# Optimization experiments

Measured on AMD Instinct MI355X. Metric: run time of the kernel, lower is better.

The kernel has to match this reference:

```python
import jax, jax.numpy as jnp
import numpy as np

B, S = 64, 200
DK = 32           # d_k = d_a = d_e
NQ = 4096         # n_question
NE = 20000        # n_exercise
NAT = 2000
NIT = 2000


def _xavier(k, shape):
    a = float(np.sqrt(6.0 / (shape[0] + shape[1])))
    return jax.random.uniform(k, shape, jnp.float32, -a, a)


def setup_inputs() -> dict:
    key = jax.random.key(0)
    ks = jax.random.split(key, 24)
    d = {}
    d['e_data'] = jax.random.randint(ks[0], (B, S), 0, NE)
    d['at_data'] = jax.random.randint(ks[1], (B, S), 0, NAT)
    d['it_data'] = jax.random.randint(ks[2], (B, S), 0, NIT)
    d['a_data'] = jax.random.randint(ks[3], (B, S), 0, 2).astype(jnp.float32)
    # binary Q-matrix: ~64 skills per exercise on average
    d['q_matrix'] = (jax.random.uniform(ks[4], (NE + 10, NQ + 1)) < (64.0 / NQ)).astype(jnp.float32)
    d['E_e'] = _xavier(ks[5], (NE + 10, DK))
    d['E_at'] = _xavier(ks[6], (NAT + 10, DK))
    d['E_it'] = _xavier(ks[7], (NIT + 10, DK))
    d['W1'] = _xavier(ks[8], (DK, 3 * DK)); d['b1'] = jnp.zeros((DK,), jnp.float32)
    d['W2'] = _xavier(ks[9], (DK, 4 * DK)); d['b2'] = jnp.zeros((DK,), jnp.float32)
    d['W3'] = _xavier(ks[10], (DK, 4 * DK)); d['b3'] = jnp.zeros((DK,), jnp.float32)
    d['W4'] = _xavier(ks[11], (DK, 3 * DK)); d['b4'] = jnp.zeros((DK,), jnp.float32)
    d['W5'] = _xavier(ks[12], (DK, 2 * DK)); d['b5'] = jnp.zeros((DK,), jnp.float32)
    d['h0'] = _xavier(ks[13], (NQ + 1, DK))
    return d


def _forward(e_data, at_data, it_data, a_data, q_matrix, E_e, E_at, E_it,
             W1, b1, W2, b2, W3, b3, W4, b4, W5, b5, h0):
    e_emb = E_e[e_data]                    # [B,S,DK]
    at_emb = E_at[at_data]                 # [B,S,DK]
    it_emb = E_it[it_data]                 # [B,S,DK]
    a_rep = jnp.broadcast_to(a_data[:, :, None], (B, S, DK))  # repeat answer to d_a
    all_learning = jnp.einsum('bsf,kf->bsk', jnp.concatenate([e_emb, at_emb, a_rep], -1), W1) + b1

    h_pre0 = jnp.broadcast_to(h0[None], (B, NQ + 1, DK))
    h_tilde0 = jnp.einsum('bn,bnd->bd', q_matrix[e_data[:, 0]], h_pre0)
    W4h, W4l, W4i = W4[:, :DK], W4[:, DK:2 * DK], W4[:, 2 * DK:]

    def step(carry, xs):
        learning_pre, h_pre, h_tilde_pre = carry
        e_t, it, learning, e_next_emb, e_next = xs
        q_e = q_matrix[e_t]                               # [B,NQ+1] gather
        x = jnp.concatenate([learning_pre, it, learning, h_tilde_pre], -1)  # [B,4DK]
        lg = jnp.tanh(x @ W2.T + b2)
        gl = jax.nn.sigmoid(x @ W3.T + b3)
        LG = gl * (lg + 1.0) * 0.5                        # [B,DK]
        LG_tilde = q_e[:, :, None] * LG[:, None, :]       # scatter (outer product), dropout off (eval)
        gamma_f = jax.nn.sigmoid(h_pre @ W4h.T + (LG @ W4l.T + it @ W4i.T + b4)[:, None, :])
        h = LG_tilde + gamma_f * h_pre                    # [B,NQ+1,DK]
        h_tilde = jnp.einsum('bn,bnd->bd', q_matrix[e_next], h)
        y = jax.nn.sigmoid(jnp.concatenate([e_next_emb, h_tilde], -1) @ W5.T + b5).sum(-1) / DK
        return (learning, h, h_tilde), y

    xs = (e_data[:, :-1].T,
          jnp.swapaxes(it_emb[:, :-1], 0, 1),
          jnp.swapaxes(all_learning[:, :-1], 0, 1),
          jnp.swapaxes(e_emb[:, 1:], 0, 1),
          e_data[:, 1:].T)
    init = (jnp.zeros((B, DK), jnp.float32), h_pre0, h_tilde0)
    _, ys = jax.lax.scan(step, init, xs)                  # ys: [S-1,B]
    pred = jnp.concatenate([jnp.zeros((B, 1), jnp.float32), ys.T], axis=1)
    return pred


def reference(e_data, at_data, it_data, a_data, q_matrix, E_e, E_at, E_it,
              W1, b1, W2, b2, W3, b3, W4, b4, W5, b5, h0):
    return _forward(e_data, at_data, it_data, a_data, q_matrix, E_e, E_at, E_it,
                    W1, b1, W2, b2, W3, b3, W4, b4, W5, b5, h0)
```

## Files before the change

kernel.cpp:

```cpp
#include <hip/hip_runtime.h>

#define Bv    64
#define Sv    200
#define DKv   32
#define NQ1v  4097
#define NWG   8
#define TPB   256
#define ROWS  2
#define NSTEP 199

typedef unsigned long long u64;

__device__ __forceinline__ float fsig(float x) {
  return __builtin_amdgcn_rcpf(1.0f + __builtin_amdgcn_exp2f(x * -1.4426950408889634f));
}
__device__ __forceinline__ float ftanh_(float x) {
  return fmaf(2.0f, fsig(2.0f * x), -1.0f);
}
__device__ __forceinline__ u64 packvt(float v, unsigned tag) {
  return ((u64)tag << 32) | (u64)__float_as_uint(v);
}

__global__ void lpkt_init(float* out) {
  int i = threadIdx.x;
  if (i < Bv) out[i * Sv] = 0.0f;
}

__global__ __launch_bounds__(TPB, 2) void lpkt_main(
    const int* __restrict__ e_data, const int* __restrict__ at_data,
    const int* __restrict__ it_data, const float* __restrict__ a_data,
    const float* __restrict__ q_matrix,
    const float* __restrict__ E_e, const float* __restrict__ E_at, const float* __restrict__ E_it,
    const float* __restrict__ W1, const float* __restrict__ b1,
    const float* __restrict__ W2, const float* __restrict__ b2,
    const float* __restrict__ W3, const float* __restrict__ b3,
    const float* __restrict__ W4, const float* __restrict__ b4,
    const float* __restrict__ W5, const float* __restrict__ b5,
    const float* __restrict__ h0, float* __restrict__ out,
    u64* __restrict__ partial)
{
  const int tid = threadIdx.x;
  const int wg  = blockIdx.x & (NWG - 1);
  const int b   = blockIdx.x / NWG;
  const int k   = tid & 31;
  const int p   = tid >> 5;
  const int nbase = wg * (TPB * ROWS);

  __shared__ __align__(16) float xw_lds[96];
  __shared__ __align__(16) float it_lds[DKv];
  __shared__ __align__(16) float lcA[DKv], lcB[DKv];
  __shared__ __align__(16) float ht_lds[DKv];
  __shared__ __align__(16) float LG_lds[DKv];
  __shared__ __align__(16) float c_lds[DKv];
  __shared__ __align__(16) float red[8][DKv];
  __shared__ __align__(16) float red2[8][DKv];
  __shared__ float ht_part[DKv];
  __shared__ __align__(16) float h49[DKv];
  __shared__ float W2T[128 * DKv];
  __shared__ float W3T[128 * DKv];

  for (int idx = tid; idx < 128 * DKv; idx += TPB) {
    int kk = idx >> 7, j = idx & 127;
    W2T[j * DKv + kk] = W2[idx];
    W3T[j * DKv + kk] = W3[idx];
  }
  if (tid < DKv) { ht_part[tid] = 0.0f; lcB[tid] = 0.0f; }
  if (wg == 0 && tid < DKv) h49[tid] = h0[4096 * DKv + tid];

  float h[ROWS][DKv];
#pragma unroll
  for (int r = 0; r < ROWS; r++) {
    const float4* hp = (const float4*)(h0 + (size_t)(nbase + r * TPB + tid) * DKv);
#pragma unroll
    for (int i = 0; i < 8; i++) {
      float4 v = hp[i];
      h[r][4*i] = v.x; h[r][4*i+1] = v.y; h[r][4*i+2] = v.z; h[r][4*i+3] = v.w;
    }
  }
  const int e0 = e_data[b * Sv];
  const float* q0 = q_matrix + (size_t)e0 * NQ1v;
  float qc[ROWS];
#pragma unroll
  for (int r = 0; r < ROWS; r++) qc[r] = q0[nbase + r * TPB + tid];
  float qc49 = (wg == 0 && tid < DKv) ? q0[4096] : 0.0f;
  __syncthreads();

#pragma unroll
  for (int r = 0; r < ROWS; r++) {
    if (qc[r] != 0.0f) {
#pragma unroll
      for (int kk = 0; kk < DKv; kk++) atomicAdd(&ht_part[kk], h[r][kk]);
    }
  }
  if (wg == 0 && tid < DKv && qc49 != 0.0f) atomicAdd(&ht_part[tid], h49[tid]);
  __syncthreads();
  if (tid < DKv)
    __hip_atomic_store(&partial[((size_t)(1 % 3) * Bv + b) * (NWG * DKv) + wg * DKv + tid],
                       packvt(ht_part[tid], 1u), __ATOMIC_RELAXED, __HIP_MEMORY_SCOPE_AGENT);

  for (int t = 0; t < NSTEP; t++) {
    float* lc_cur  = (t & 1) ? lcB : lcA;
    float* lc_prev = (t & 1) ? lcA : lcB;
    const unsigned tau_g = (unsigned)(t + 1);
    const unsigned tau_p = (unsigned)(t + 2);

    const int ecur  = e_data[b * Sv + t];
    const int enext = e_data[b * Sv + t + 1];
    const int atc   = at_data[b * Sv + t];
    const int itc   = it_data[b * Sv + t];
    const float av  = a_data[b * Sv + t];
    const float* qnr = q_matrix + (size_t)enext * NQ1v;
    float qn[ROWS];
#pragma unroll
    for (int r = 0; r < ROWS; r++) qn[r] = qnr[nbase + r * TPB + tid];
    float qn49 = (wg == 0 && tid < DKv) ? qnr[4096] : 0.0f;

    if (tid < 96)
      xw_lds[tid] = (tid < 32) ? E_e[(size_t)ecur * DKv + tid]
                  : (tid < 64) ? E_at[(size_t)atc * DKv + (tid - 32)] : av;
    else if (tid < 128)
      it_lds[tid - 96] = E_it[(size_t)itc * DKv + (tid - 96)];

    float acc[ROWS][DKv];
#pragma unroll
    for (int kk = 0; kk < DKv; kk++) {
      float a0 = 0.0f, a1 = 0.0f;
#pragma unroll
      for (int d = 0; d < DKv; d += 4) {
        float4 w = *(const float4*)&W4[kk * 96 + d];
        a0 = fmaf(w.x, h[0][d+0], a0); a1 = fmaf(w.x, h[1][d+0], a1);
        a0 = fmaf(w.y, h[0][d+1], a0); a1 = fmaf(w.y, h[1][d+1], a1);
        a0 = fmaf(w.z, h[0][d+2], a0); a1 = fmaf(w.z, h[1][d+2], a1);
        a0 = fmaf(w.w, h[0][d+3], a0); a1 = fmaf(w.w, h[1][d+3], a1);
      }
      acc[0][kk] = a0; acc[1][kk] = a1;
    }
    __syncthreads();

    if (tid >= 32 && tid < 64) {
      const int kx = tid - 32;
      float s = b1[kx];
      const float4* wp = (const float4*)&W1[kx * 96];
      const float4* xp = (const float4*)xw_lds;
#pragma unroll
      for (int i = 0; i < 24; i++) {
        float4 w = wp[i]; float4 x = xp[i];
        s = fmaf(x.x, w.x, s); s = fmaf(x.y, w.y, s);
        s = fmaf(x.z, w.z, s); s = fmaf(x.w, w.w, s);
      }
      lc_cur[kx] = s;
    }
    if (tid < DKv) {
      const u64* pb = partial + ((size_t)(tau_g % 3) * Bv + b) * (NWG * DKv) + tid;
      u64 v[NWG];
      for (;;) {
        bool ok = true;
#pragma unroll
        for (int w2 = 0; w2 < NWG; w2++) {
          v[w2] = __hip_atomic_load(&pb[w2 * DKv], __ATOMIC_RELAXED, __HIP_MEMORY_SCOPE_AGENT);
          ok = ok && ((unsigned)(v[w2] >> 32) == tau_g);
        }
        if (ok) break;
        __builtin_amdgcn_s_sleep(2);
      }
      float s = 0.0f;
#pragma unroll
      for (int w2 = 0; w2 < NWG; w2++) s += __uint_as_float((unsigned)v[w2]);
      ht_lds[tid] = s;
    }
    __syncthreads();

    {
      const int seg = p >> 1;
      const float* sp = (seg == 0) ? lc_prev : (seg == 1) ? it_lds
                      : (seg == 2) ? lc_cur  : ht_lds;
      const int off = (p & 1) * 16;
      float xv[16];
#pragma unroll
      for (int i = 0; i < 4; i++) {
        float4 v = ((const float4*)(sp + off))[i];
        xv[4*i] = v.x; xv[4*i+1] = v.y; xv[4*i+2] = v.z; xv[4*i+3] = v.w;
      }
      float s2 = 0.0f, s3 = 0.0f;
      const int jb = 16 * p;
#pragma unroll
      for (int i = 0; i < 16; i++) {
        s2 = fmaf(xv[i], W2T[(jb + i) * DKv + k], s2);
        s3 = fmaf(xv[i], W3T[(jb + i) * DKv + k], s3);
      }
      red[p][k] = s2; red2[p][k] = s3;
    }
    __syncthreads();

    if (tid < DKv) {
      float s2 = b2[tid], s3 = b3[tid];
#pragma unroll
      for (int pp = 0; pp < 8; pp++) { s2 += red[pp][tid]; s3 += red2[pp][tid]; }
      LG_lds[tid] = fsig(s3) * (ftanh_(s2) + 1.0f) * 0.5f;
    } else if (tid < 64) ht_part[tid - 32] = 0.0f;
    __syncthreads();

    {
      const float* up = (p < 4) ? (LG_lds + 8 * p) : (it_lds + 8 * (p - 4));
      const float4* wp = (const float4*)&W4[k * 96 + 32 + 8 * p];
      float4 w0 = wp[0], w1 = wp[1];
      float pc = 0.0f;
      pc = fmaf(up[0], w0.x, pc); pc = fmaf(up[1], w0.y, pc);
      pc = fmaf(up[2], w0.z, pc); pc = fmaf(up[3], w0.w, pc);
      pc = fmaf(up[4], w1.x, pc); pc = fmaf(up[5], w1.y, pc);
      pc = fmaf(up[6], w1.z, pc); pc = fmaf(up[7], w1.w, pc);
      red[p][k] = pc;
    }
    if (wg == 0 && t >= 1 && tid >= 64 && tid < 128) {
      const int p2 = p - 2;
      const float* zs = (p2 == 0) ? xw_lds : ht_lds;
      const float4* wp = (const float4*)&W5[k * 64 + 32 * p2];
      float acc5 = 0.0f;
#pragma unroll
      for (int i = 0; i < 8; i++) {
        float4 w = wp[i]; float4 z = ((const float4*)zs)[i];
        acc5 = fmaf(z.x, w.x, acc5); acc5 = fmaf(z.y, w.y, acc5);
        acc5 = fmaf(z.z, w.z, acc5); acc5 = fmaf(z.w, w.w, acc5);
      }
      red2[p2][k] = acc5;
    }
    __syncthreads();

    if (tid < DKv) {
      float s = b4[tid];
#pragma unroll
      for (int pp = 0; pp < 8; pp++) s += red[pp][tid];
      c_lds[tid] = s;
    } else if (wg == 0 && t >= 1 && tid < 64) {
      const int kx = tid - 32;
      float s = fsig(b5[kx] + red2[0][kx] + red2[1][kx]);
#pragma unroll
      for (int m = 1; m < 32; m <<= 1) s += __shfl_xor(s, m);
      if (tid == 32) out[b * Sv + t] = s * (1.0f / DKv);
    }
    __syncthreads();

    {
      float c_r[DKv], lg_r[DKv];
#pragma unroll
      for (int i = 0; i < 8; i++) {
        float4 cv = ((const float4*)c_lds)[i];
        float4 gv = ((const float4*)LG_lds)[i];
        c_r[4*i] = cv.x; c_r[4*i+1] = cv.y; c_r[4*i+2] = cv.z; c_r[4*i+3] = cv.w;
        lg_r[4*i] = gv.x; lg_r[4*i+1] = gv.y; lg_r[4*i+2] = gv.z; lg_r[4*i+3] = gv.w;
      }
#pragma unroll
      for (int r = 0; r < ROWS; r++) {
        const float qcr = qc[r];
#pragma unroll
        for (int kk = 0; kk < DKv; kk++) {
          float g = fsig(acc[r][kk] + c_r[kk]);
          h[r][kk] = fmaf(g, h[r][kk], qcr * lg_r[kk]);
        }
        if (qn[r] != 0.0f) {
#pragma unroll
          for (int kk = 0; kk < DKv; kk++) atomicAdd(&ht_part[kk], h[r][kk]);
        }
        qc[r] = qn[r];
      }
    }
    if (wg == 0 && tid < DKv) {
      float hh[DKv];
#pragma unroll
      for (int i = 0; i < 8; i++) {
        float4 v = ((const float4*)h49)[i];
        hh[4*i] = v.x; hh[4*i+1] = v.y; hh[4*i+2] = v.z; hh[4*i+3] = v.w;
      }
      float a = c_lds[tid];
#pragma unroll
      for (int d = 0; d < DKv; d += 4) {
        float4 w = *(const float4*)&W4[tid * 96 + d];
        a = fmaf(w.x, hh[d+0], a); a = fmaf(w.y, hh[d+1], a);
        a = fmaf(w.z, hh[d+2], a); a = fmaf(w.w, hh[d+3], a);
      }
      float hn = fmaf(fsig(a), h49[tid], qc49 * LG_lds[tid]);
      h49[tid] = hn;
      if (qn49 != 0.0f) atomicAdd(&ht_part[tid], hn);
      qc49 = qn49;
    }
    __syncthreads();

    if (tid < DKv)
      __hip_atomic_store(&partial[((size_t)(tau_p % 3) * Bv + b) * (NWG * DKv) + wg * DKv + tid],
                         packvt(ht_part[tid], tau_p), __ATOMIC_RELAXED, __HIP_MEMORY_SCOPE_AGENT);
  }

  if (wg == 0) {
    const unsigned tau_f = (unsigned)(NSTEP + 1);
    if (tid < DKv) {
      const u64* pb = partial + ((size_t)(tau_f % 3) * Bv + b) * (NWG * DKv) + tid;
      u64 v[NWG];
      for (;;) {
        bool ok = true;
#pragma unroll
        for (int w2 = 0; w2 < NWG; w2++) {
          v[w2] = __hip_atomic_load(&pb[w2 * DKv], __ATOMIC_RELAXED, __HIP_MEMORY_SCOPE_AGENT);
          ok = ok && ((unsigned)(v[w2] >> 32) == tau_f);
        }
        if (ok) break;
        __builtin_amdgcn_s_sleep(2);
      }
      float s = 0.0f;
#pragma unroll
      for (int w2 = 0; w2 < NWG; w2++) s += __uint_as_float((unsigned)v[w2]);
      ht_lds[tid] = s;
      xw_lds[tid] = E_e[(size_t)e_data[b * Sv + 199] * DKv + tid];
    }
    __syncthreads();
    if (tid >= 64 && tid < 128) {
      const int p2 = p - 2;
      const float* zs = (p2 == 0) ? xw_lds : ht_lds;
      const float4* wp = (const float4*)&W5[k * 64 + 32 * p2];
      float acc5 = 0.0f;
#pragma unroll
      for (int i = 0; i < 8; i++) {
        float4 w = wp[i]; float4 z = ((const float4*)zs)[i];
        acc5 = fmaf(z.x, w.x, acc5); acc5 = fmaf(z.y, w.y, acc5);
        acc5 = fmaf(z.z, w.z, acc5); acc5 = fmaf(z.w, w.w, acc5);
      }
      red2[p2][k] = acc5;
    }
    __syncthreads();
    if (tid >= 32 && tid < 64) {
      const int kx = tid - 32;
      float s = fsig(b5[kx] + red2[0][kx] + red2[1][kx]);
#pragma unroll
      for (int m = 1; m < 32; m <<= 1) s += __shfl_xor(s, m);
      if (tid == 32) out[b * Sv + 199] = s * (1.0f / DKv);
    }
  }
}

extern "C" void kernel_launch(void* const* d_in, const int* in_sizes, int n_in,
                              void* d_out, int out_size, void* d_ws, size_t ws_size,
                              hipStream_t stream) {
  const int*   e_data   = (const int*)d_in[0];
  const int*   at_data  = (const int*)d_in[1];
  const int*   it_data  = (const int*)d_in[2];
  const float* a_data   = (const float*)d_in[3];
  const float* q_matrix = (const float*)d_in[4];
  const float* E_e      = (const float*)d_in[5];
  const float* E_at     = (const float*)d_in[6];
  const float* E_it     = (const float*)d_in[7];
  const float* W1 = (const float*)d_in[8];
  const float* b1 = (const float*)d_in[9];
  const float* W2 = (const float*)d_in[10];
  const float* b2 = (const float*)d_in[11];
  const float* W3 = (const float*)d_in[12];
  const float* b3 = (const float*)d_in[13];
  const float* W4 = (const float*)d_in[14];
  const float* b4 = (const float*)d_in[15];
  const float* W5 = (const float*)d_in[16];
  const float* b5 = (const float*)d_in[17];
  const float* h0 = (const float*)d_in[18];
  float* out = (float*)d_out;

  u64* partial = (u64*)d_ws;

  lpkt_init<<<1, 64, 0, stream>>>(out);
  lpkt_main<<<dim3(Bv * NWG), dim3(TPB), 0, stream>>>(
      e_data, at_data, it_data, a_data, q_matrix, E_e, E_at, E_it,
      W1, b1, W2, b2, W3, b3, W4, b4, W5, b5, h0, out, partial);
}
```

Before: 5.190 ms.

## Cache weights in LDS, use atomic RMW for cross-block flags, split warp roles

```diff
diff --git a/kernel.cpp b/kernel.cpp
--- a/kernel.cpp
+++ b/kernel.cpp
@@ -19,6 +19,12 @@
 }
 __device__ __forceinline__ u64 packvt(float v, unsigned tag) {
   return ((u64)tag << 32) | (u64)__float_as_uint(v);
+}
+__device__ __forceinline__ u64 fresh_read(u64* p) {
+  return __hip_atomic_fetch_add(p, 0ull, __ATOMIC_RELAXED, __HIP_MEMORY_SCOPE_AGENT);
+}
+__device__ __forceinline__ void fresh_write(u64* p, u64 v) {
+  (void)__hip_atomic_exchange(p, v, __ATOMIC_RELAXED, __HIP_MEMORY_SCOPE_AGENT);
 }
 
 __global__ void lpkt_init(float* out) {
@@ -46,6 +52,11 @@
   const int p   = tid >> 5;
   const int nbase = wg * (TPB * ROWS);
 
+  __shared__ float W23T[128 * 64];
+  __shared__ __align__(16) float W1L[32 * 100];
+  __shared__ __align__(16) float W4L[32 * 100];
+  __shared__ __align__(16) float W5L[32 * 68];
+  __shared__ float bL[5 * 32];
   __shared__ __align__(16) float xw_lds[96];
   __shared__ __align__(16) float it_lds[DKv];
   __shared__ __align__(16) float lcA[DKv], lcB[DKv];
@@ -56,13 +67,25 @@
   __shared__ __align__(16) float red2[8][DKv];
   __shared__ float ht_part[DKv];
   __shared__ __align__(16) float h49[DKv];
-  __shared__ float W2T[128 * DKv];
-  __shared__ float W3T[128 * DKv];
-
-  for (int idx = tid; idx < 128 * DKv; idx += TPB) {
-    int kk = idx >> 7, j = idx & 127;
-    W2T[j * DKv + kk] = W2[idx];
-    W3T[j * DKv + kk] = W3[idx];
+
+  for (int idx = tid; idx < 128 * 32; idx += TPB) {
+    int j = idx & 127, kk = idx >> 7;
+    W23T[j * 64 + 2 * kk]     = W2[kk * 128 + j];
+    W23T[j * 64 + 2 * kk + 1] = W3[kk * 128 + j];
+  }
+  for (int idx = tid; idx < 32 * 96; idx += TPB) {
+    int r = idx / 96, c = idx % 96;
+    W1L[r * 100 + c] = W1[idx];
+    W4L[r * 100 + c] = W4[idx];
+  }
+  for (int idx = tid; idx < 32 * 64; idx += TPB) {
+    int r = idx >> 6, c = idx & 63;
+    W5L[r * 68 + c] = W5[idx];
+  }
+  if (tid < 32) {
+    bL[0 * 32 + tid] = b1[tid]; bL[1 * 32 + tid] = b2[tid];
+    bL[2 * 32 + tid] = b3[tid]; bL[3 * 32 + tid] = b4[tid];
+    bL[4 * 32 + tid] = b5[tid];
   }
   if (tid < DKv) { ht_part[tid] = 0.0f; lcB[tid] = 0.0f; }
   if (wg == 0 && tid < DKv) h49[tid] = h0[4096 * DKv + tid];
@@ -95,8 +118,8 @@
   if (wg == 0 && tid < DKv && qc49 != 0.0f) atomicAdd(&ht_part[tid], h49[tid]);
   __syncthreads();
   if (tid < DKv)
-    __hip_atomic_store(&partial[((size_t)(1 % 3) * Bv + b) * (NWG * DKv) + wg * DKv + tid],
-                       packvt(ht_part[tid], 1u), __ATOMIC_RELAXED, __HIP_MEMORY_SCOPE_AGENT);
+    fresh_write(&partial[((size_t)(1 % 3) * Bv + b) * (NWG * DKv) + wg * DKv + tid],
+                packvt(ht_part[tid], 1u));
 
   for (int t = 0; t < NSTEP; t++) {
     float* lc_cur  = (t & 1) ? lcB : lcA;
@@ -137,10 +160,27 @@
     }
     __syncthreads();
 
-    if (tid >= 32 && tid < 64) {
-      const int kx = tid - 32;
-      float s = b1[kx];
-      const float4* wp = (const float4*)&W1[kx * 96];
+    if (tid < DKv) {
+      u64* pb = partial + ((size_t)(tau_g % 3) * Bv + b) * (NWG * DKv) + tid;
+      u64 v[NWG];
+      for (;;) {
+        bool ok = true;
+#pragma unroll
+        for (int w2 = 0; w2 < NWG; w2++) {
+          v[w2] = fresh_read(&pb[w2 * DKv]);
+          ok = ok && ((unsigned)(v[w2] >> 32) == tau_g);
+        }
+        if (ok) break;
+        __builtin_amdgcn_s_sleep(2);
+      }
+      float s = 0.0f;
+#pragma unroll
+      for (int w2 = 0; w2 < NWG; w2++) s += __uint_as_float((unsigned)v[w2]);
+      ht_lds[tid] = s;
+    } else if (tid >= 64 && tid < 96) {
+      const int kx = tid - 64;
+      float s = bL[0 * 32 + kx];
+      const float4* wp = (const float4*)&W1L[kx * 100];
       const float4* xp = (const float4*)xw_lds;
 #pragma unroll
       for (int i = 0; i < 24; i++) {
@@ -149,24 +189,6 @@
         s = fmaf(x.z, w.z, s); s = fmaf(x.w, w.w, s);
       }
       lc_cur[kx] = s;
-    }
-    if (tid < DKv) {
-      const u64* pb = partial + ((size_t)(tau_g % 3) * Bv + b) * (NWG * DKv) + tid;
-      u64 v[NWG];
-      for (;;) {
-        bool ok = true;
-#pragma unroll
-        for (int w2 = 0; w2 < NWG; w2++) {
-          v[w2] = __hip_atomic_load(&pb[w2 * DKv], __ATOMIC_RELAXED, __HIP_MEMORY_SCOPE_AGENT);
-          ok = ok && ((unsigned)(v[w2] >> 32) == tau_g);
-        }
-        if (ok) break;
-        __builtin_amdgcn_s_sleep(2);
-      }
-      float s = 0.0f;
-#pragma unroll
-      for (int w2 = 0; w2 < NWG; w2++) s += __uint_as_float((unsigned)v[w2]);
-      ht_lds[tid] = s;
     }
     __syncthreads();
 
@@ -185,24 +207,25 @@
       const int jb = 16 * p;
 #pragma unroll
       for (int i = 0; i < 16; i++) {
-        s2 = fmaf(xv[i], W2T[(jb + i) * DKv + k], s2);
-        s3 = fmaf(xv[i], W3T[(jb + i) * DKv + k], s3);
+        float2 w = *(const float2*)&W23T[(jb + i) * 64 + 2 * k];
+        s2 = fmaf(xv[i], w.x, s2);
+        s3 = fmaf(xv[i], w.y, s3);
       }
       red[p][k] = s2; red2[p][k] = s3;
     }
     __syncthreads();
 
     if (tid < DKv) {
-      float s2 = b2[tid], s3 = b3[tid];
+      float s2 = bL[1 * 32 + tid], s3 = bL[2 * 32 + tid];
 #pragma unroll
       for (int pp = 0; pp < 8; pp++) { s2 += red[pp][tid]; s3 += red2[pp][tid]; }
       LG_lds[tid] = fsig(s3) * (ftanh_(s2) + 1.0f) * 0.5f;
-    } else if (tid < 64) ht_part[tid - 32] = 0.0f;
+    } else if (tid >= 128 && tid < 160) ht_part[tid - 128] = 0.0f;
     __syncthreads();
 
     {
       const float* up = (p < 4) ? (LG_lds + 8 * p) : (it_lds + 8 * (p - 4));
-      const float4* wp = (const float4*)&W4[k * 96 + 32 + 8 * p];
+      const float4* wp = (const float4*)&W4L[k * 100 + 32 + 8 * p];
       float4 w0 = wp[0], w1 = wp[1];
       float pc = 0.0f;
       pc = fmaf(up[0], w0.x, pc); pc = fmaf(up[1], w0.y, pc);
@@ -214,7 +237,7 @@
     if (wg == 0 && t >= 1 && tid >= 64 && tid < 128) {
       const int p2 = p - 2;
       const float* zs = (p2 == 0) ? xw_lds : ht_lds;
-      const float4* wp = (const float4*)&W5[k * 64 + 32 * p2];
+      const float4* wp = (const float4*)&W5L[k * 68 + 32 * p2];
       float acc5 = 0.0f;
 #pragma unroll
       for (int i = 0; i < 8; i++) {
@@ -227,16 +250,16 @@
     __syncthreads();
 
     if (tid < DKv) {
-      float s = b4[tid];
+      float s = bL[3 * 32 + tid];
 #pragma unroll
       for (int pp = 0; pp < 8; pp++) s += red[pp][tid];
       c_lds[tid] = s;
-    } else if (wg == 0 && t >= 1 && tid < 64) {
-      const int kx = tid - 32;
-      float s = fsig(b5[kx] + red2[0][kx] + red2[1][kx]);
+    } else if (wg == 0 && t >= 1 && tid >= 96 && tid < 128) {
+      const int kx = tid - 96;
+      float s = fsig(bL[4 * 32 + kx] + red2[0][kx] + red2[1][kx]);
 #pragma unroll
       for (int m = 1; m < 32; m <<= 1) s += __shfl_xor(s, m);
-      if (tid == 32) out[b * Sv + t] = s * (1.0f / DKv);
+      if (tid == 96) out[b * Sv + t] = s * (1.0f / DKv);
     }
     __syncthreads();
 
@@ -274,7 +297,7 @@
       float a = c_lds[tid];
 #pragma unroll
       for (int d = 0; d < DKv; d += 4) {
-        float4 w = *(const float4*)&W4[tid * 96 + d];
+        float4 w = *(const float4*)&W4L[tid * 100 + d];
         a = fmaf(w.x, hh[d+0], a); a = fmaf(w.y, hh[d+1], a);
         a = fmaf(w.z, hh[d+2], a); a = fmaf(w.w, hh[d+3], a);
       }
@@ -286,20 +309,20 @@
     __syncthreads();
 
     if (tid < DKv)
-      __hip_atomic_store(&partial[((size_t)(tau_p % 3) * Bv + b) * (NWG * DKv) + wg * DKv + tid],
-                         packvt(ht_part[tid], tau_p), __ATOMIC_RELAXED, __HIP_MEMORY_SCOPE_AGENT);
+      fresh_write(&partial[((size_t)(tau_p % 3) * Bv + b) * (NWG * DKv) + wg * DKv + tid],
+                  packvt(ht_part[tid], tau_p));
   }
 
   if (wg == 0) {
     const unsigned tau_f = (unsigned)(NSTEP + 1);
     if (tid < DKv) {
-      const u64* pb = partial + ((size_t)(tau_f % 3) * Bv + b) * (NWG * DKv) + tid;
+      u64* pb = partial + ((size_t)(tau_f % 3) * Bv + b) * (NWG * DKv) + tid;
       u64 v[NWG];
       for (;;) {
         bool ok = true;
 #pragma unroll
         for (int w2 = 0; w2 < NWG; w2++) {
-          v[w2] = __hip_atomic_load(&pb[w2 * DKv], __ATOMIC_RELAXED, __HIP_MEMORY_SCOPE_AGENT);
+          v[w2] = fresh_read(&pb[w2 * DKv]);
           ok = ok && ((unsigned)(v[w2] >> 32) == tau_f);
         }
         if (ok) break;
@@ -315,7 +338,7 @@
     if (tid >= 64 && tid < 128) {
       const int p2 = p - 2;
       const float* zs = (p2 == 0) ? xw_lds : ht_lds;
-      const float4* wp = (const float4*)&W5[k * 64 + 32 * p2];
+      const float4* wp = (const float4*)&W5L[k * 68 + 32 * p2];
       float acc5 = 0.0f;
 #pragma unroll
       for (int i = 0; i < 8; i++) {
@@ -326,12 +349,12 @@
       red2[p2][k] = acc5;
     }
     __syncthreads();
-    if (tid >= 32 && tid < 64) {
-      const int kx = tid - 32;
-      float s = fsig(b5[kx] + red2[0][kx] + red2[1][kx]);
+    if (tid >= 96 && tid < 128) {
+      const int kx = tid - 96;
+      float s = fsig(bL[4 * 32 + kx] + red2[0][kx] + red2[1][kx]);
 #pragma unroll
       for (int m = 1; m < 32; m <<= 1) s += __shfl_xor(s, m);
-      if (tid == 32) out[b * Sv + 199] = s * (1.0f / DKv);
+      if (tid == 96) out[b * Sv + 199] = s * (1.0f / DKv);
     }
   }
 }
```

After: 4.904 ms. 1.06x faster.

## Restructure recurrent step: 512 threads, one row each, single-wave small matmuls

Applied to the files above, without the earlier changes.

```diff
diff --git a/kernel.cpp b/kernel.cpp
--- a/kernel.cpp
+++ b/kernel.cpp
@@ -5,8 +5,7 @@
 #define DKv   32
 #define NQ1v  4097
 #define NWG   8
-#define TPB   256
-#define ROWS  2
+#define TPB   512
 #define NSTEP 199
 
 typedef unsigned long long u64;
@@ -19,6 +18,12 @@
 }
 __device__ __forceinline__ u64 packvt(float v, unsigned tag) {
   return ((u64)tag << 32) | (u64)__float_as_uint(v);
+}
+__device__ __forceinline__ u64 fresh_read(u64* p) {
+  return __hip_atomic_fetch_add(p, 0ull, __ATOMIC_RELAXED, __HIP_MEMORY_SCOPE_AGENT);
+}
+__device__ __forceinline__ void fresh_write(u64* p, u64 v) {
+  (void)__hip_atomic_exchange(p, v, __ATOMIC_RELAXED, __HIP_MEMORY_SCOPE_AGENT);
 }
 
 __global__ void lpkt_init(float* out) {
@@ -26,7 +31,7 @@
   if (i < Bv) out[i * Sv] = 0.0f;
 }
 
-__global__ __launch_bounds__(TPB, 2) void lpkt_main(
+__global__ __launch_bounds__(TPB, 4) void lpkt_main(
     const int* __restrict__ e_data, const int* __restrict__ at_data,
     const int* __restrict__ it_data, const float* __restrict__ a_data,
     const float* __restrict__ q_matrix,
@@ -39,300 +44,241 @@
     const float* __restrict__ h0, float* __restrict__ out,
     u64* __restrict__ partial)
 {
-  const int tid = threadIdx.x;
-  const int wg  = blockIdx.x & (NWG - 1);
-  const int b   = blockIdx.x / NWG;
-  const int k   = tid & 31;
-  const int p   = tid >> 5;
-  const int nbase = wg * (TPB * ROWS);
-
-  __shared__ __align__(16) float xw_lds[96];
-  __shared__ __align__(16) float it_lds[DKv];
-  __shared__ __align__(16) float lcA[DKv], lcB[DKv];
-  __shared__ __align__(16) float ht_lds[DKv];
-  __shared__ __align__(16) float LG_lds[DKv];
-  __shared__ __align__(16) float c_lds[DKv];
-  __shared__ __align__(16) float red[8][DKv];
-  __shared__ __align__(16) float red2[8][DKv];
-  __shared__ float ht_part[DKv];
+  const int tid  = threadIdx.x;
+  const int b    = blockIdx.x & 63;
+  const int wg   = blockIdx.x >> 6;
+  const int lane = tid & 63;
+  const int wave = tid >> 6;
+  const int row  = wg * TPB + tid;
+
+  __shared__ float W2T[128 * 33], W3T[128 * 33];
+  __shared__ float W1T[96 * 33];
+  __shared__ float W4cT[64 * 33];
+  __shared__ float W4hT[32 * 33];
+  __shared__ float W5T[64 * 33];
+  __shared__ float bs[5 * 32];
+  __shared__ __align__(16) float lc_s[2][DKv];
+  __shared__ __align__(16) float ht_s[DKv];
+  __shared__ __align__(16) float LG_s[DKv], c_s[DKv];
+  __shared__ __align__(16) float ht_part[2][DKv];
   __shared__ __align__(16) float h49[DKv];
-  __shared__ float W2T[128 * DKv];
-  __shared__ float W3T[128 * DKv];
-
-  for (int idx = tid; idx < 128 * DKv; idx += TPB) {
-    int kk = idx >> 7, j = idx & 127;
-    W2T[j * DKv + kk] = W2[idx];
-    W3T[j * DKv + kk] = W3[idx];
-  }
-  if (tid < DKv) { ht_part[tid] = 0.0f; lcB[tid] = 0.0f; }
+
+  for (int idx = tid; idx < 128 * 32; idx += TPB) {
+    int i = idx & 127, j = idx >> 7;
+    W2T[i * 33 + j] = W2[j * 128 + i];
+    W3T[i * 33 + j] = W3[j * 128 + i];
+  }
+  for (int idx = tid; idx < 32 * 96; idx += TPB) {
+    int j = idx / 96, d = idx % 96;
+    W1T[d * 33 + j] = W1[idx];
+    float v = W4[idx];
+    if (d < 32) W4hT[d * 33 + j] = v;
+    else        W4cT[(d - 32) * 33 + j] = v;
+  }
+  for (int idx = tid; idx < 32 * 64; idx += TPB) {
+    int j = idx >> 6, i = idx & 63;
+    W5T[i * 33 + j] = W5[idx];
+  }
+  if (tid < 32) {
+    bs[tid] = b1[tid]; bs[32 + tid] = b2[tid]; bs[64 + tid] = b3[tid];
+    bs[96 + tid] = b4[tid]; bs[128 + tid] = b5[tid];
+    ht_part[0][tid] = 0.0f; ht_part[1][tid] = 0.0f;
+    lc_s[0][tid] = 0.0f; lc_s[1][tid] = 0.0f;
+  }
   if (wg == 0 && tid < DKv) h49[tid] = h0[4096 * DKv + tid];
 
-  float h[ROWS][DKv];
-#pragma unroll
-  for (int r = 0; r < ROWS; r++) {
-    const float4* hp = (const float4*)(h0 + (size_t)(nbase + r * TPB + tid) * DKv);
+  float h[DKv];
+  {
+    const float4* hp = (const float4*)(h0 + (size_t)row * DKv);
 #pragma unroll
     for (int i = 0; i < 8; i++) {
       float4 v = hp[i];
-      h[r][4*i] = v.x; h[r][4*i+1] = v.y; h[r][4*i+2] = v.z; h[r][4*i+3] = v.w;
-    }
-  }
-  const int e0 = e_data[b * Sv];
-  const float* q0 = q_matrix + (size_t)e0 * NQ1v;
-  float qc[ROWS];
-#pragma unroll
-  for (int r = 0; r < ROWS; r++) qc[r] = q0[nbase + r * TPB + tid];
-  float qc49 = (wg == 0 && tid < DKv) ? q0[4096] : 0.0f;
+      h[4*i] = v.x; h[4*i+1] = v.y; h[4*i+2] = v.z; h[4*i+3] = v.w;
+    }
+  }
+  float qc = q_matrix[(size_t)e_data[b * Sv] * NQ1v + row];
+  float qc49 = 0.0f;
+  if (wg == 0 && wave == 0 && lane < DKv)
+    qc49 = q_matrix[(size_t)e_data[b * Sv] * NQ1v + 4096];
   __syncthreads();
 
-#pragma unroll
-  for (int r = 0; r < ROWS; r++) {
-    if (qc[r] != 0.0f) {
-#pragma unroll
-      for (int kk = 0; kk < DKv; kk++) atomicAdd(&ht_part[kk], h[r][kk]);
-    }
-  }
-  if (wg == 0 && tid < DKv && qc49 != 0.0f) atomicAdd(&ht_part[tid], h49[tid]);
+  if (qc != 0.0f) {
+#pragma unroll
+    for (int kk = 0; kk < DKv; kk++) atomicAdd(&ht_part[1][kk], h[kk]);
+  }
+  if (wg == 0 && wave == 0 && lane < DKv && qc49 != 0.0f)
+    atomicAdd(&ht_part[1][lane], h49[lane]);
   __syncthreads();
-  if (tid < DKv)
-    __hip_atomic_store(&partial[((size_t)(1 % 3) * Bv + b) * (NWG * DKv) + wg * DKv + tid],
-                       packvt(ht_part[tid], 1u), __ATOMIC_RELAXED, __HIP_MEMORY_SCOPE_AGENT);
+  if (wave == 0 && lane < DKv) {
+    fresh_write(&partial[((size_t)(1 % 3) * Bv + b) * (NWG * DKv) + wg * DKv + lane],
+                packvt(ht_part[1][lane], 1u));
+    ht_part[1][lane] = 0.0f;
+  }
 
   for (int t = 0; t < NSTEP; t++) {
-    float* lc_cur  = (t & 1) ? lcB : lcA;
-    float* lc_prev = (t & 1) ? lcA : lcB;
+    const int par = t & 1;
     const unsigned tau_g = (unsigned)(t + 1);
     const unsigned tau_p = (unsigned)(t + 2);
 
-    const int ecur  = e_data[b * Sv + t];
-    const int enext = e_data[b * Sv + t + 1];
-    const int atc   = at_data[b * Sv + t];
-    const int itc   = it_data[b * Sv + t];
-    const float av  = a_data[b * Sv + t];
-    const float* qnr = q_matrix + (size_t)enext * NQ1v;
-    float qn[ROWS];
-#pragma unroll
-    for (int r = 0; r < ROWS; r++) qn[r] = qnr[nbase + r * TPB + tid];
-    float qn49 = (wg == 0 && tid < DKv) ? qnr[4096] : 0.0f;
-
-    if (tid < 96)
-      xw_lds[tid] = (tid < 32) ? E_e[(size_t)ecur * DKv + tid]
-                  : (tid < 64) ? E_at[(size_t)atc * DKv + (tid - 32)] : av;
-    else if (tid < 128)
-      it_lds[tid - 96] = E_it[(size_t)itc * DKv + (tid - 96)];
-
-    float acc[ROWS][DKv];
+    const int ec  = e_data[b * Sv + t];
+    const int atc = at_data[b * Sv + t];
+    const int itc = it_data[b * Sv + t];
+    const float av = a_data[b * Sv + t];
+    const float* eerow = E_e  + (size_t)ec  * DKv;
+    const float* atrow = E_at + (size_t)atc * DKv;
+    const float* itrow = E_it + (size_t)itc * DKv;
+
+    const float* qnr = q_matrix + (size_t)e_data[b * Sv + t + 1] * NQ1v;
+    float qn = qnr[row];
+    float qn49 = 0.0f;
+    if (wg == 0 && wave == 0 && lane < DKv) qn49 = qnr[4096];
+
+    float acc[DKv];
 #pragma unroll
     for (int kk = 0; kk < DKv; kk++) {
-      float a0 = 0.0f, a1 = 0.0f;
+      float a = 0.0f;
 #pragma unroll
       for (int d = 0; d < DKv; d += 4) {
         float4 w = *(const float4*)&W4[kk * 96 + d];
-        a0 = fmaf(w.x, h[0][d+0], a0); a1 = fmaf(w.x, h[1][d+0], a1);
-        a0 = fmaf(w.y, h[0][d+1], a0); a1 = fmaf(w.y, h[1][d+1], a1);
-        a0 = fmaf(w.z, h[0][d+2], a0); a1 = fmaf(w.z, h[1][d+2], a1);
-        a0 = fmaf(w.w, h[0][d+3], a0); a1 = fmaf(w.w, h[1][d+3], a1);
+        a = fmaf(w.x, h[d+0], a); a = fmaf(w.y, h[d+1], a);
+        a = fmaf(w.z, h[d+2], a); a = fmaf(w.w, h[d+3], a);
       }
-      acc[0][kk] = a0; acc[1][kk] = a1;
+      acc[kk] = a;
+    }
+
+    if (wave == 0) {
+      if (lane < 32) {
+        u64* pb = partial + ((size_t)(tau_g % 3) * Bv + b) * (NWG * DKv) + lane;
+        u64 v[NWG];
+        for (;;) {
+          bool ok = true;
+#pragma unroll
+          for (int w2 = 0; w2 < NWG; w2++) {
+            v[w2] = fresh_read(&pb[w2 * DKv]);
+            ok = ok && ((unsigned)(v[w2] >> 32) == tau_g);
+          }
+          if (ok) break;
+          __builtin_amdgcn_s_sleep(2);
+        }
+        float s = 0.0f;
+#pragma unroll
+        for (int w2 = 0; w2 < NWG; w2++) s += __uint_as_float((unsigned)v[w2]);
+        ht_s[lane] = s;
+      } else {
+        const int jx = lane - 32;
+        float s = bs[jx];
+#pragma unroll
+        for (int i = 0; i < 32; i++) s = fmaf(eerow[i], W1T[i * 33 + jx], s);
+#pragma unroll
+        for (int i = 0; i < 32; i++) s = fmaf(atrow[i], W1T[(32 + i) * 33 + jx], s);
+#pragma unroll
+        for (int i = 0; i < 32; i++) s = fmaf(av,       W1T[(64 + i) * 33 + jx], s);
+        lc_s[par][jx] = s;
+      }
     }
     __syncthreads();
 
-    if (tid >= 32 && tid < 64) {
-      const int kx = tid - 32;
-      float s = b1[kx];
-      const float4* wp = (const float4*)&W1[kx * 96];
-      const float4* xp = (const float4*)xw_lds;
-#pragma unroll
-      for (int i = 0; i < 24; i++) {
-        float4 w = wp[i]; float4 x = xp[i];
-        s = fmaf(x.x, w.x, s); s = fmaf(x.y, w.y, s);
-        s = fmaf(x.z, w.z, s); s = fmaf(x.w, w.w, s);
+    float LGreg = 0.0f, creg = 0.0f;
+    if (wave == 0) {
+      const int jx = lane & 31;
+      float s = (lane < 32) ? bs[32 + jx] : bs[64 + jx];
+      const float* WT = (lane < 32) ? W2T : W3T;
+#pragma unroll
+      for (int i = 0; i < 32; i++) s = fmaf(lc_s[1 - par][i], WT[i * 33 + jx], s);
+#pragma unroll
+      for (int i = 0; i < 32; i++) s = fmaf(itrow[i],         WT[(32 + i) * 33 + jx], s);
+#pragma unroll
+      for (int i = 0; i < 32; i++) s = fmaf(lc_s[par][i],     WT[(64 + i) * 33 + jx], s);
+#pragma unroll
+      for (int i = 0; i < 32; i++) s = fmaf(ht_s[i],          WT[(96 + i) * 33 + jx], s);
+      float v = (lane < 32) ? ftanh_(s) : fsig(s);
+      float pr = __shfl_xor(v, 32);
+      LGreg = (lane < 32) ? pr * (v + 1.0f) * 0.5f : v * (pr + 1.0f) * 0.5f;
+      if (lane < 32) {
+        LG_s[lane] = LGreg;
+        float c = bs[96 + lane];
+#pragma unroll
+        for (int d = 0; d < 32; d++)
+          c = fmaf(__shfl(LGreg, d), W4cT[d * 33 + lane], c);
+#pragma unroll
+        for (int d = 0; d < 32; d++)
+          c = fmaf(itrow[d], W4cT[(32 + d) * 33 + lane], c);
+        creg = c; c_s[lane] = c;
+      } else if (wg == 0 && t >= 1) {
+        float y = bs[128 + jx];
+#pragma unroll
+        for (int i = 0; i < 32; i++) y = fmaf(eerow[i], W5T[i * 33 + jx], y);
+#pragma unroll
+        for (int i = 0; i < 32; i++) y = fmaf(ht_s[i],  W5T[(32 + i) * 33 + jx], y);
+        y = fsig(y);
+#pragma unroll
+        for (int m = 1; m < 32; m <<= 1) y += __shfl_xor(y, m);
+        if (lane == 32) out[b * Sv + t] = y * (1.0f / DKv);
       }
-      lc_cur[kx] = s;
-    }
-    if (tid < DKv) {
-      const u64* pb = partial + ((size_t)(tau_g % 3) * Bv + b) * (NWG * DKv) + tid;
-      u64 v[NWG];
-      for (;;) {
-        bool ok = true;
-#pragma unroll
-        for (int w2 = 0; w2 < NWG; w2++) {
-          v[w2] = __hip_atomic_load(&pb[w2 * DKv], __ATOMIC_RELAXED, __HIP_MEMORY_SCOPE_AGENT);
-          ok = ok && ((unsigned)(v[w2] >> 32) == tau_g);
-        }
-        if (ok) break;
-        __builtin_amdgcn_s_sleep(2);
+    }
+    __syncthreads();
+
+#pragma unroll
+    for (int kk = 0; kk < DKv; kk++) {
+      float g = fsig(acc[kk] + c_s[kk]);
+      h[kk] = fmaf(g, h[kk], qc * LG_s[kk]);
+    }
+    if (qn != 0.0f) {
+#pragma unroll
+      for (int kk = 0; kk < DKv; kk++) atomicAdd(&ht_part[par][kk], h[kk]);
+    }
+    qc = qn;
+    if (wg == 0 && wave == 0 && lane < DKv) {
+      float a = creg;
+#pragma unroll
+      for (int d = 0; d < DKv; d++) a = fmaf(W4hT[d * 33 + lane], h49[d], a);
+      float hold = h49[lane];
+      float hn = fmaf(fsig(a), hold, qc49 * LGreg);
+      h49[lane] = hn;
+      if (qn49 != 0.0f) atomicAdd(&ht_part[par][lane], hn);
+      qc49 = qn49;
+    }
+    __syncthreads();
+
+    if (wave == 0 && lane < DKv) {
+      fresh_write(&partial[((size_t)(tau_p % 3) * Bv + b) * (NWG * DKv) + wg * DKv + lane],
+                  packvt(ht_part[par][lane], tau_p));
+      ht_part[par][lane] = 0.0f;
+    }
+  }
+
+  if (wg == 0 && wave == 0 && lane < 32) {
+    const unsigned tau_f = (unsigned)(NSTEP + 1);
+    u64* pb = partial + ((size_t)(tau_f % 3) * Bv + b) * (NWG * DKv) + lane;
+    u64 v[NWG];
+    for (;;) {
+      bool ok = true;
+#pragma unroll
+      for (int w2 = 0; w2 < NWG; w2++) {
+        v[w2] = fresh_read(&pb[w2 * DKv]);
+        ok = ok && ((unsigned)(v[w2] >> 32) == tau_f);
       }
-      float s = 0.0f;
-#pragma unroll
-      for (int w2 = 0; w2 < NWG; w2++) s += __uint_as_float((unsigned)v[w2]);
-      ht_lds[tid] = s;
-    }
-    __syncthreads();
-
-    {
-      const int seg = p >> 1;
-      const float* sp = (seg == 0) ? lc_prev : (seg == 1) ? it_lds
-                      : (seg == 2) ? lc_cur  : ht_lds;
-      const int off = (p & 1) * 16;
-      float xv[16];
-#pragma unroll
-      for (int i = 0; i < 4; i++) {
-        float4 v = ((const float4*)(sp + off))[i];
-        xv[4*i] = v.x; xv[4*i+1] = v.y; xv[4*i+2] = v.z; xv[4*i+3] = v.w;
-      }
-      float s2 = 0.0f, s3 = 0.0f;
-      const int jb = 16 * p;
-#pragma unroll
-      for (int i = 0; i < 16; i++) {
-        s2 = fmaf(xv[i], W2T[(jb + i) * DKv + k], s2);
-        s3 = fmaf(xv[i], W3T[(jb + i) * DKv + k], s3);
-      }
-      red[p][k] = s2; red2[p][k] = s3;
-    }
-    __syncthreads();
-
-    if (tid < DKv) {
-      float s2 = b2[tid], s3 = b3[tid];
-#pragma unroll
-      for (int pp = 0; pp < 8; pp++) { s2 += red[pp][tid]; s3 += red2[pp][tid]; }
-      LG_lds[tid] = fsig(s3) * (ftanh_(s2) + 1.0f) * 0.5f;
-    } else if (tid < 64) ht_part[tid - 32] = 0.0f;
-    __syncthreads();
-
-    {
-      const float* up = (p < 4) ? (LG_lds + 8 * p) : (it_lds + 8 * (p - 4));
-      const float4* wp = (const float4*)&W4[k * 96 + 32 + 8 * p];
-      float4 w0 = wp[0], w1 = wp[1];
-      float pc = 0.0f;
-      pc = fmaf(up[0], w0.x, pc); pc = fmaf(up[1], w0.y, pc);
-      pc = fmaf(up[2], w0.z, pc); pc = fmaf(up[3], w0.w, pc);
-      pc = fmaf(up[4], w1.x, pc); pc = fmaf(up[5], w1.y, pc);
-      pc = fmaf(up[6], w1.z, pc); pc = fmaf(up[7], w1.w, pc);
-      red[p][k] = pc;
-    }
-    if (wg == 0 && t >= 1 && tid >= 64 && tid < 128) {
-      const int p2 = p - 2;
-      const float* zs = (p2 == 0) ? xw_lds : ht_lds;
-      const float4* wp = (const float4*)&W5[k * 64 + 32 * p2];
-      float acc5 = 0.0f;
-#pragma unroll
-      for (int i = 0; i < 8; i++) {
-        float4 w = wp[i]; float4 z = ((const float4*)zs)[i];
-        acc5 = fmaf(z.x, w.x, acc5); acc5 = fmaf(z.y, w.y, acc5);
-        acc5 = fmaf(z.z, w.z, acc5); acc5 = fmaf(z.w, w.w, acc5);
-      }
-      red2[p2][k] = acc5;
-    }
-    __syncthreads();
-
-    if (tid < DKv) {
-      float s = b4[tid];
-#pragma unroll
-      for (int pp = 0; pp < 8; pp++) s += red[pp][tid];
-      c_lds[tid] = s;
-    } else if (wg == 0 && t >= 1 && tid < 64) {
-      const int kx = tid - 32;
-      float s = fsig(b5[kx] + red2[0][kx] + red2[1][kx]);
-#pragma unroll
-      for (int m = 1; m < 32; m <<= 1) s += __shfl_xor(s, m);
-      if (tid == 32) out[b * Sv + t] = s * (1.0f / DKv);
-    }
-    __syncthreads();
-
-    {
-      float c_r[DKv], lg_r[DKv];
-#pragma unroll
-      for (int i = 0; i < 8; i++) {
-        float4 cv = ((const float4*)c_lds)[i];
-        float4 gv = ((const float4*)LG_lds)[i];
-        c_r[4*i] = cv.x; c_r[4*i+1] = cv.y; c_r[4*i+2] = cv.z; c_r[4*i+3] = cv.w;
-        lg_r[4*i] = gv.x; lg_r[4*i+1] = gv.y; lg_r[4*i+2] = gv.z; lg_r[4*i+3] = gv.w;
-      }
-#pragma unroll
-      for (int r = 0; r < ROWS; r++) {
-        const float qcr = qc[r];
-#pragma unroll
-        for (int kk = 0; kk < DKv; kk++) {
-          float g = fsig(acc[r][kk] + c_r[kk]);
-          h[r][kk] = fmaf(g, h[r][kk], qcr * lg_r[kk]);
-        }
-        if (qn[r] != 0.0f) {
-#pragma unroll
-          for (int kk = 0; kk < DKv; kk++) atomicAdd(&ht_part[kk], h[r][kk]);
-        }
-        qc[r] = qn[r];
-      }
-    }
-    if (wg == 0 && tid < DKv) {
-      float hh[DKv];
-#pragma unroll
-      for (int i = 0; i < 8; i++) {
-        float4 v = ((const float4*)h49)[i];
-        hh[4*i] = v.x; hh[4*i+1] = v.y; hh[4*i+2] = v.z; hh[4*i+3] = v.w;
-      }
-      float a = c_lds[tid];
-#pragma unroll
-      for (int d = 0; d < DKv; d += 4) {
-        float4 w = *(const float4*)&W4[tid * 96 + d];
-        a = fmaf(w.x, hh[d+0], a); a = fmaf(w.y, hh[d+1], a);
-        a = fmaf(w.z, hh[d+2], a); a = fmaf(w.w, hh[d+3], a);
-      }
-      float hn = fmaf(fsig(a), h49[tid], qc49 * LG_lds[tid]);
-      h49[tid] = hn;
-      if (qn49 != 0.0f) atomicAdd(&ht_part[tid], hn);
-      qc49 = qn49;
-    }
-    __syncthreads();
-
-    if (tid < DKv)
-      __hip_atomic_store(&partial[((size_t)(tau_p % 3) * Bv + b) * (NWG * DKv) + wg * DKv + tid],
-                         packvt(ht_part[tid], tau_p), __ATOMIC_RELAXED, __HIP_MEMORY_SCOPE_AGENT);
-  }
-
-  if (wg == 0) {
-    const unsigned tau_f = (unsigned)(NSTEP + 1);
-    if (tid < DKv) {
-      const u64* pb = partial + ((size_t)(tau_f % 3) * Bv + b) * (NWG * DKv) + tid;
-      u64 v[NWG];
-      for (;;) {
-        bool ok = true;
-#pragma unroll
-        for (int w2 = 0; w2 < NWG; w2++) {
-          v[w2] = __hip_atomic_load(&pb[w2 * DKv], __ATOMIC_RELAXED, __HIP_MEMORY_SCOPE_AGENT);
-          ok = ok && ((unsigned)(v[w2] >> 32) == tau_f);
-        }
-        if (ok) break;
-        __builtin_amdgcn_s_sleep(2);
-      }
-      float s = 0.0f;
-#pragma unroll
-      for (int w2 = 0; w2 < NWG; w2++) s += __uint_as_float((unsigned)v[w2]);
-      ht_lds[tid] = s;
-      xw_lds[tid] = E_e[(size_t)e_data[b * Sv + 199] * DKv + tid];
-    }
-    __syncthreads();
-    if (tid >= 64 && tid < 128) {
-      const int p2 = p - 2;
-      const float* zs = (p2 == 0) ? xw_lds : ht_lds;
-      const float4* wp = (const float4*)&W5[k * 64 + 32 * p2];
-      float acc5 = 0.0f;
-#pragma unroll
-      for (int i = 0; i < 8; i++) {
-        float4 w = wp[i]; float4 z = ((const float4*)zs)[i];
-        acc5 = fmaf(z.x, w.x, acc5); acc5 = fmaf(z.y, w.y, acc5);
-        acc5 = fmaf(z.z, w.z, acc5); acc5 = fmaf(z.w, w.w, acc5);
-      }
-      red2[p2][k] = acc5;
-    }
-    __syncthreads();
-    if (tid >= 32 && tid < 64) {
-      const int kx = tid - 32;
-      float s = fsig(b5[kx] + red2[0][kx] + red2[1][kx]);
-#pragma unroll
-      for (int m = 1; m < 32; m <<= 1) s += __shfl_xor(s, m);
-      if (tid == 32) out[b * Sv + 199] = s * (1.0f / DKv);
-    }
+      if (ok) break;
+      __builtin_amdgcn_s_sleep(2);
+    }
+    float s = 0.0f;
+#pragma unroll
+    for (int w2 = 0; w2 < NWG; w2++) s += __uint_as_float((unsigned)v[w2]);
+    ht_s[lane] = s;
+  }
+  __syncthreads();
+  if (wg == 0 && wave == 0 && lane >= 32) {
+    const int jx = lane - 32;
+    const float* enrow = E_e + (size_t)e_data[b * Sv + NSTEP] * DKv;
+    float y = bs[128 + jx];
+#pragma unroll
+    for (int i = 0; i < 32; i++) y = fmaf(enrow[i], W5T[i * 33 + jx], y);
+#pragma unroll
+    for (int i = 0; i < 32; i++) y = fmaf(ht_s[i],  W5T[(32 + i) * 33 + jx], y);
+    y = fsig(y);
+#pragma unroll
+    for (int m = 1; m < 32; m <<= 1) y += __shfl_xor(y, m);
+    if (lane == 32) out[b * Sv + NSTEP] = y * (1.0f / DKv);
   }
 }
 
```

New measurement: 6.397 ms. 23.3% more time.
